# Kernel tuning notes

Hardware: AMD Instinct MI355X
Metric: run time of the kernel (lower is better)

The kernel has to match this reference:

```python
import jax, jax.numpy as jnp
import numpy as np

B, T, N, E = 4, 8, 512, 8192
CIN, H, HEADS = 64, 128, 4


def setup_inputs() -> dict:
    key = jax.random.key(0)
    ks = jax.random.split(key, 8)
    G = B * T
    s = 0.05
    return {
        "x": jax.random.normal(ks[0], (G, N, CIN), jnp.float32),
        "edge_index": jax.random.randint(ks[1], (G, 2, E), 0, N, dtype=jnp.int64),
        "W1": jax.random.normal(ks[2], (CIN, H), jnp.float32) * s,
        "b1": jnp.zeros((H,), jnp.float32),
        "W2": jax.random.normal(ks[3], (H, H), jnp.float32) * s,
        "b2": jnp.zeros((H,), jnp.float32),
        "in_proj_w": jax.random.normal(ks[4], (3 * H, H), jnp.float32) * s,
        "in_proj_b": jnp.zeros((3 * H,), jnp.float32),
        "out_proj_w": jax.random.normal(ks[5], (H, H), jnp.float32) * s,
        "out_proj_b": jnp.zeros((H,), jnp.float32),
    }


def gcn_layer(x, src, dst, W, b, num_nodes):
    # PyG GCNConv: add self-loops, sym-normalize deg^-1/2[src]*deg^-1/2[dst]
    xl = x @ W                                            # [GN, H]
    deg = jax.ops.segment_sum(jnp.ones_like(dst, dtype=xl.dtype), dst,
                              num_segments=num_nodes) + 1.0  # +1 self-loop
    dinv = jax.lax.rsqrt(deg)
    norm = dinv[src] * dinv[dst]                          # [Etot]
    agg = jax.ops.segment_sum(xl[src] * norm[:, None], dst, num_segments=num_nodes)
    agg = agg + xl * (dinv * dinv)[:, None]               # self-loop term
    return agg + b


def reference(x, edge_index, W1, b1, W2, b2, in_proj_w, in_proj_b, out_proj_w, out_proj_b):
    G, n, cin = x.shape
    GN = G * n
    offs = (jnp.arange(G, dtype=edge_index.dtype) * n)[:, None]  # disjoint union
    src = (edge_index[:, 0, :] + offs).reshape(-1)
    dst = (edge_index[:, 1, :] + offs).reshape(-1)
    xf = x.reshape(GN, cin)
    h = gcn_layer(xf, src, dst, W1, b1, GN)
    h = gcn_layer(h, src, dst, W2, b2, GN)
    hc = h.shape[-1]
    h = h.reshape(B, T * n, hc)                           # [B, S, H]
    # torch.nn.MultiheadAttention with packed qkv in_proj
    qkv = h @ in_proj_w.T + in_proj_b
    q, k, v = jnp.split(qkv, 3, axis=-1)
    hd = hc // HEADS
    def sh(t):
        return t.reshape(B, -1, HEADS, hd).transpose(0, 2, 1, 3)  # [B,h,S,d]
    q, k, v = sh(q), sh(k), sh(v)
    att = jax.nn.softmax(jnp.einsum('bhqd,bhkd->bhqk', q, k) / jnp.sqrt(jnp.float32(hd)), axis=-1)
    o = jnp.einsum('bhqk,bhkd->bhqd', att, v).transpose(0, 2, 1, 3).reshape(B, -1, hc)
    return o @ out_proj_w.T + out_proj_b
```

## Files before the change

### kernel.cpp

```cpp
#include <hip/hip_runtime.h>
#include <hip/hip_bf16.h>

#define G     32
#define NPG   512
#define EPG   8192
#define GN    16384
#define ETOT  (G*EPG)
#define CIN   64
#define H     128
#define NB    4
#define S     4096
#define HEADS 4
#define HD    32
#define QKV   384

typedef __attribute__((ext_vector_type(8))) short short8;
typedef __attribute__((ext_vector_type(4))) float floatx4;

__device__ __forceinline__ float bf16_to_f32(unsigned short u) {
    unsigned int x = ((unsigned int)u) << 16;
    return __uint_as_float(x);
}
__device__ __forceinline__ unsigned short f32_to_bf16(float f) {
    __hip_bfloat16 h = (__hip_bfloat16)f;
    return *(unsigned short*)&h;
}
__device__ __forceinline__ float ldf(const void* p, long i, int f32) {
    return f32 ? ((const float*)p)[i] : bf16_to_f32(((const unsigned short*)p)[i]);
}

__global__ void detect_kernel(const unsigned short* __restrict__ xraw,
                              const int* __restrict__ eiraw, int* __restrict__ flags) {
    __shared__ float smax[256];
    __shared__ int   sor[256];
    int t = threadIdx.x;
    float m = 0.f;
    for (int i = t; i < 4096; i += 256)
        m = fmaxf(m, fabsf(bf16_to_f32(xraw[i])));
    int orv = 0;
    for (int i = t; i < 2048; i += 256)
        orv |= eiraw[2 * i + 1];
    smax[t] = m; sor[t] = orv;
    __syncthreads();
    for (int off = 128; off > 0; off >>= 1) {
        if (t < off) {
            smax[t] = fmaxf(smax[t], smax[t + off]);
            sor[t] |= sor[t + off];
        }
        __syncthreads();
    }
    if (t == 0) {
        flags[0] = (smax[0] > 1000.f) ? 1 : 0;
        flags[1] = (sor[0] == 0) ? 1 : 0;
    }
}

#define XN   (GN*CIN)
#define E1   (XN + H*CIN)
#define E2   (E1 + H*H)
#define E3   (E2 + QKV*H)
#define E4   (E3 + H*H)
#define E5   (E4 + H)
#define E6   (E5 + H)
#define E7   (E6 + QKV)
#define CTOT (E7 + H)
__global__ void conv_all_kernel(const void* x_raw, const void* W1_raw, const void* b1_raw,
                                const void* W2_raw, const void* b2_raw, const void* Wq_raw,
                                const void* bq_raw, const void* Wo_raw, const void* bo_raw,
                                unsigned short* __restrict__ xb,
                                unsigned short* __restrict__ W1T,
                                unsigned short* __restrict__ W2T,
                                unsigned short* __restrict__ Wqb,
                                unsigned short* __restrict__ Wob,
                                float* __restrict__ b1f, float* __restrict__ b2f,
                                float* __restrict__ bqf, float* __restrict__ bof,
                                const int* __restrict__ flags) {
    int i = blockIdx.x * blockDim.x + threadIdx.x;
    if (i >= CTOT) return;
    int f32 = flags[0];
    if (i < XN) {
        xb[i] = f32_to_bf16(ldf(x_raw, i, f32));
    } else if (i < E1) {
        int j = i - XN, c = j / CIN, r = j - c * CIN;
        W1T[j] = f32_to_bf16(ldf(W1_raw, (long)r * H + c, f32));
    } else if (i < E2) {
        int j = i - E1, c = j >> 7, r = j & 127;
        W2T[j] = f32_to_bf16(ldf(W2_raw, (long)r * H + c, f32));
    } else if (i < E3) {
        int j = i - E2;
        Wqb[j] = f32_to_bf16(ldf(Wq_raw, j, f32));
    } else if (i < E4) {
        int j = i - E3;
        Wob[j] = f32_to_bf16(ldf(Wo_raw, j, f32));
    } else if (i < E5) { b1f[i - E4] = ldf(b1_raw, i - E4, f32); }
    else if (i < E6) { b2f[i - E5] = ldf(b2_raw, i - E5, f32); }
    else if (i < E7) { bqf[i - E6] = ldf(bq_raw, i - E6, f32); }
    else             { bof[i - E7] = ldf(bo_raw, i - E7, f32); }
}

__global__ void edges_kernel(const int* __restrict__ ei, int* __restrict__ srcA,
                             int* __restrict__ dstA, const int* __restrict__ flags) {
    int t = blockIdx.x * blockDim.x + threadIdx.x;
    if (t >= ETOT) return;
    int g = t >> 13, e = t & (EPG - 1);
    int sh = flags[1];
    long long si = ((long long)(g * 2 + 0) * EPG + e) << sh;
    long long di = ((long long)(g * 2 + 1) * EPG + e) << sh;
    srcA[t] = g * NPG + ei[si];
    dstA[t] = g * NPG + ei[di];
}

__global__ void count_kernel(const int* __restrict__ dstA, int* __restrict__ cnt) {
    int t = blockIdx.x * blockDim.x + threadIdx.x;
    if (t >= ETOT) return;
    atomicAdd(&cnt[dstA[t]], 1);
}

__global__ void scan_kernel(const int* __restrict__ cnt, int* __restrict__ row_start,
                            int* __restrict__ fill_pos, float* __restrict__ dinv) {
    __shared__ int tmp[NPG];
    int g = blockIdx.x, t = threadIdx.x;
    int c = cnt[g * NPG + t];
    tmp[t] = c;
    __syncthreads();
    for (int off = 1; off < NPG; off <<= 1) {
        int v = (t >= off) ? tmp[t - off] : 0;
        __syncthreads();
        tmp[t] += v;
        __syncthreads();
    }
    int excl = tmp[t] - c;
    int rs = g * EPG + excl;
    row_start[g * NPG + t] = rs;
    fill_pos[g * NPG + t]  = rs;
    dinv[g * NPG + t] = 1.0f / sqrtf((float)c + 1.0f);
}

__global__ void fill_kernel(const int* __restrict__ srcA, const int* __restrict__ dstA,
                            int* __restrict__ fill_pos, int* __restrict__ csr_src) {
    int t = blockIdx.x * blockDim.x + threadIdx.x;
    if (t >= ETOT) return;
    int pos = atomicAdd(&fill_pos[dstA[t]], 1);
    csr_src[pos] = srcA[t];
}

template<int KD>
__global__ __launch_bounds__(256) void mm_gcn_kernel(const unsigned short* __restrict__ A,
        const unsigned short* __restrict__ B, const float* __restrict__ dinv,
        unsigned short* __restrict__ Y) {
    int tid = threadIdx.x, wave = tid >> 6, lane = tid & 63, m = lane & 15, quad = lane >> 4;
    int row0 = blockIdx.x * 64 + wave * 16;
    floatx4 acc[8] = {};
    for (int kc = 0; kc < KD; kc += 32) {
        short8 af = *(const short8*)&A[(size_t)(row0 + m) * KD + kc + quad * 8];
#pragma unroll
        for (int t = 0; t < 8; t++) {
            short8 bf = *(const short8*)&B[(size_t)(t * 16 + m) * KD + kc + quad * 8];
            acc[t] = __builtin_amdgcn_mfma_f32_16x16x32_bf16(af, bf, acc[t], 0, 0, 0);
        }
    }
    int rbase = row0 + quad * 4;
    float4 dv4 = *(const float4*)&dinv[rbase];
    float dv[4] = {dv4.x, dv4.y, dv4.z, dv4.w};
#pragma unroll
    for (int t = 0; t < 8; t++) {
        int col = t * 16 + m;
#pragma unroll
        for (int r = 0; r < 4; r++)
            Y[(size_t)(rbase + r) * H + col] = f32_to_bf16(acc[t][r] * dv[r]);
    }
}

__global__ void agg_kernel(const unsigned short* __restrict__ y,
                           const int* __restrict__ row_start, const int* __restrict__ cnt,
                           const int* __restrict__ csr_src, const float* __restrict__ dinv,
                           const float* __restrict__ bias, unsigned short* __restrict__ hout) {
    int i = blockIdx.x;
    int c = threadIdx.x;
    float acc = bf16_to_f32(y[(size_t)i * H + c]);
    int rs = row_start[i], n = cnt[i];
    int p = 0;
    for (; p + 4 <= n; p += 4) {
        int s0 = csr_src[rs + p + 0];
        int s1 = csr_src[rs + p + 1];
        int s2 = csr_src[rs + p + 2];
        int s3 = csr_src[rs + p + 3];
        float a0 = bf16_to_f32(y[(size_t)s0 * H + c]);
        float a1 = bf16_to_f32(y[(size_t)s1 * H + c]);
        float a2 = bf16_to_f32(y[(size_t)s2 * H + c]);
        float a3 = bf16_to_f32(y[(size_t)s3 * H + c]);
        acc += (a0 + a1) + (a2 + a3);
    }
    for (; p < n; p++)
        acc += bf16_to_f32(y[(size_t)csr_src[rs + p] * H + c]);
    hout[(size_t)i * H + c] = f32_to_bf16(acc * dinv[i] + bias[c]);
}

__global__ __launch_bounds__(256) void mmqkv_kernel(const unsigned short* __restrict__ A,
        const unsigned short* __restrict__ B, const float* __restrict__ bias,
        unsigned short* __restrict__ Qx, unsigned short* __restrict__ Kx,
        unsigned short* __restrict__ Vtx) {
    int tid = threadIdx.x, wave = tid >> 6, lane = tid & 63, m = lane & 15, quad = lane >> 4;
    int row0 = blockIdx.x * 64 + wave * 16;
    floatx4 acc[24] = {};
    for (int kc = 0; kc < H; kc += 32) {
        short8 af = *(const short8*)&A[(size_t)(row0 + m) * H + kc + quad * 8];
#pragma unroll
        for (int t = 0; t < 24; t++) {
            short8 bf = *(const short8*)&B[(size_t)(t * 16 + m) * H + kc + quad * 8];
            acc[t] = __builtin_amdgcn_mfma_f32_16x16x32_bf16(af, bf, acc[t], 0, 0, 0);
        }
    }
    int rbase = row0 + quad * 4;
    int b = rbase >> 12, s0 = rbase & (S - 1);
#pragma unroll
    for (int t = 0; t < 24; t++) {
        int j = t * 16 + m;
        float bj = bias[j];
        int jj = j & 127, head = jj >> 5, hd = jj & 31;
        int bh = b * HEADS + head;
        if (t < 8) {
#pragma unroll
            for (int r = 0; r < 4; r++)
                Qx[((size_t)bh * S + s0 + r) * HD + hd] =
                    f32_to_bf16((acc[t][r] + bj) *
                                (0.17677669529663687f * 1.4426950408889634f));
        } else if (t < 16) {
#pragma unroll
            for (int r = 0; r < 4; r++)
                Kx[((size_t)bh * S + s0 + r) * HD + hd] = f32_to_bf16(acc[t][r] + bj);
        } else {
#pragma unroll
            for (int r = 0; r < 4; r++)
                Vtx[((size_t)bh * HD + hd) * S + s0 + r] = f32_to_bf16(acc[t][r] + bj);
        }
    }
}

__global__ __launch_bounds__(256) void attn7_kernel(
        const unsigned short* __restrict__ Qx, const unsigned short* __restrict__ Kx,
        const unsigned short* __restrict__ Vtx, unsigned short* __restrict__ Ob) {
    int tid = threadIdx.x, wave = tid >> 6, lane = tid & 63;
    int m = lane & 15, quad = lane >> 4;

    int n = blockIdx.x;
    int id = (n & 7) * 32 + (n >> 3);
    int tile = id & 15, bh = id >> 4;

    const unsigned short* Qb  = Qx  + (size_t)bh * S * HD;
    const unsigned short* Kb  = Kx  + (size_t)bh * S * HD;
    const unsigned short* Vtb = Vtx + (size_t)bh * HD * S;

    int q0 = tile * 256 + wave * 64;
    short8 q[4];
#pragma unroll
    for (int t = 0; t < 4; t++)
        q[t] = *(const short8*)&Qb[(size_t)(q0 + t * 16 + m) * HD + quad * 8];

    floatx4 o0[4] = {}, o1[4] = {}, l[4] = {};

    short8 ones = {16256, 16256, 16256, 16256, 16256, 16256, 16256, 16256};
    union PW { unsigned int u[4]; short8 s8; };

    short8 kf0 = *(const short8*)&Kb[(size_t)m * HD + quad * 8];
    short8 kf1 = *(const short8*)&Kb[(size_t)(m + 16) * HD + quad * 8];
    short8 vc0 = *(const short8*)&Vtb[(size_t)m * S + quad * 8];
    short8 vc1 = *(const short8*)&Vtb[(size_t)(m + 16) * S + quad * 8];

    for (int i = 0; i < S / 32; i++) {
        floatx4 z = {};
        floatx4 t0[4], t1[4];
#pragma unroll
        for (int t = 0; t < 4; t++) {
            t0[t] = __builtin_amdgcn_mfma_f32_16x16x32_bf16(kf0, q[t], z, 0, 0, 0);
            t1[t] = __builtin_amdgcn_mfma_f32_16x16x32_bf16(kf1, q[t], z, 0, 0, 0);
        }
        int ktn = ((i + 1) * 32) & (S - 1);
        kf0 = *(const short8*)&Kb[(size_t)(ktn + m) * HD + quad * 8];
        kf1 = *(const short8*)&Kb[(size_t)(ktn + m + 16) * HD + quad * 8];

        PW pw[4];
#pragma unroll
        for (int t = 0; t < 4; t++) {
            float e0 = __builtin_amdgcn_exp2f(t0[t][0]);
            float e1 = __builtin_amdgcn_exp2f(t0[t][1]);
            float e2 = __builtin_amdgcn_exp2f(t0[t][2]);
            float e3 = __builtin_amdgcn_exp2f(t0[t][3]);
            float e4 = __builtin_amdgcn_exp2f(t1[t][0]);
            float e5 = __builtin_amdgcn_exp2f(t1[t][1]);
            float e6 = __builtin_amdgcn_exp2f(t1[t][2]);
            float e7 = __builtin_amdgcn_exp2f(t1[t][3]);
            unsigned int w0, w1, w2, w3;
            asm("v_cvt_pk_bf16_f32 %0, %1, %2" : "=v"(w0) : "v"(e0), "v"(e1));
            asm("v_cvt_pk_bf16_f32 %0, %1, %2" : "=v"(w1) : "v"(e2), "v"(e3));
            asm("v_cvt_pk_bf16_f32 %0, %1, %2" : "=v"(w2) : "v"(e4), "v"(e5));
            asm("v_cvt_pk_bf16_f32 %0, %1, %2" : "=v"(w3) : "v"(e6), "v"(e7));
            asm("v_permlane32_swap_b32 %0, %1" : "+v"(w0), "+v"(w2));
            asm("v_permlane32_swap_b32 %0, %1" : "+v"(w1), "+v"(w3));
            asm("v_permlane16_swap_b32 %0, %1" : "+v"(w0), "+v"(w2));
            asm("v_permlane16_swap_b32 %0, %1" : "+v"(w1), "+v"(w3));
            pw[t].u[0] = w0; pw[t].u[1] = w1; pw[t].u[2] = w2; pw[t].u[3] = w3;
        }

#pragma unroll
        for (int t = 0; t < 4; t++) {
            o0[t] = __builtin_amdgcn_mfma_f32_16x16x32_bf16(pw[t].s8, vc0, o0[t], 0, 0, 0);
            o1[t] = __builtin_amdgcn_mfma_f32_16x16x32_bf16(pw[t].s8, vc1, o1[t], 0, 0, 0);
            l[t]  = __builtin_amdgcn_mfma_f32_16x16x32_bf16(pw[t].s8, ones, l[t], 0, 0, 0);
        }
        vc0 = *(const short8*)&Vtb[(size_t)m * S + ktn + quad * 8];
        vc1 = *(const short8*)&Vtb[(size_t)(m + 16) * S + ktn + quad * 8];
    }

    int batch = bh >> 2, head = bh & 3;
    int col = head * HD + m;
#pragma unroll
    for (int t = 0; t < 4; t++) {
        int grow = batch * S + q0 + t * 16 + quad * 4;
#pragma unroll
        for (int r = 0; r < 4; r++) {
            float inv = 1.f / l[t][r];
            Ob[(size_t)(grow + r) * H + col]      = f32_to_bf16(o0[t][r] * inv);
            Ob[(size_t)(grow + r) * H + col + 16] = f32_to_bf16(o1[t][r] * inv);
        }
    }
}

__global__ __launch_bounds__(256) void mmout_kernel(const unsigned short* __restrict__ A,
        const unsigned short* __restrict__ B, const float* __restrict__ bias,
        void* __restrict__ out, const int* __restrict__ flags) {
    int tid = threadIdx.x, wave = tid >> 6, lane = tid & 63, m = lane & 15, quad = lane >> 4;
    int row0 = blockIdx.x * 64 + wave * 16;
    floatx4 acc[8] = {};
    for (int kc = 0; kc < H; kc += 32) {
        short8 af = *(const short8*)&A[(size_t)(row0 + m) * H + kc + quad * 8];
#pragma unroll
        for (int t = 0; t < 8; t++) {
            short8 bf = *(const short8*)&B[(size_t)(t * 16 + m) * H + kc + quad * 8];
            acc[t] = __builtin_amdgcn_mfma_f32_16x16x32_bf16(af, bf, acc[t], 0, 0, 0);
        }
    }
    int rbase = row0 + quad * 4;
    int f32o = flags[0];
#pragma unroll
    for (int t = 0; t < 8; t++) {
        int col = t * 16 + m;
        float bj = bias[col];
#pragma unroll
        for (int r = 0; r < 4; r++) {
            float v = acc[t][r] + bj;
            if (f32o) ((float*)out)[(size_t)(rbase + r) * H + col] = v;
            else ((unsigned short*)out)[(size_t)(rbase + r) * H + col] = f32_to_bf16(v);
        }
    }
}

extern "C" void kernel_launch(void* const* d_in, const int* in_sizes, int n_in,
                              void* d_out, int out_size, void* d_ws, size_t ws_size,
                              hipStream_t stream) {
    const void* x_raw    = d_in[0];
    const int*  ei_raw   = (const int*)d_in[1];
    const void* W1_raw   = d_in[2];
    const void* b1_raw   = d_in[3];
    const void* W2_raw   = d_in[4];
    const void* b2_raw   = d_in[5];
    const void* Wq_raw   = d_in[6];
    const void* bq_raw   = d_in[7];
    const void* Wo_raw   = d_in[8];
    const void* bo_raw   = d_in[9];

    char* ws = (char*)d_ws;
    size_t o = 0;
    auto alloc = [&](size_t bytes) { void* p = ws + o; o += (bytes + 1023) & ~1023ull; return p; };

    int*   flags     = (int*)  alloc(1024);
    int*   cnt       = (int*)  alloc((size_t)GN * 4);
    int*   row_start = (int*)  alloc((size_t)GN * 4);
    int*   fill_pos  = (int*)  alloc((size_t)GN * 4);
    float* dinv      = (float*)alloc((size_t)GN * 4);
    int*   srcA      = (int*)  alloc((size_t)ETOT * 4);
    int*   dstA      = (int*)  alloc((size_t)ETOT * 4);
    int*   csr_src   = (int*)  alloc((size_t)ETOT * 4);
    unsigned short* xb   = (unsigned short*)alloc((size_t)GN * CIN * 2);
    unsigned short* W1T  = (unsigned short*)alloc((size_t)H * CIN * 2);
    unsigned short* W2T  = (unsigned short*)alloc((size_t)H * H * 2);
    unsigned short* Wqb  = (unsigned short*)alloc((size_t)QKV * H * 2);
    unsigned short* Wob  = (unsigned short*)alloc((size_t)H * H * 2);
    float* b1f = (float*)alloc(H * 4);
    float* b2f = (float*)alloc(H * 4);
    float* bqf = (float*)alloc(QKV * 4);
    float* bof = (float*)alloc(H * 4);
    unsigned short* y_bf = (unsigned short*)alloc((size_t)GN * H * 2);
    unsigned short* h_bf = (unsigned short*)alloc((size_t)GN * H * 2);
    unsigned short* Qx   = (unsigned short*)alloc((size_t)16 * S * HD * 2);
    unsigned short* Kx   = (unsigned short*)alloc((size_t)16 * S * HD * 2);
    unsigned short* Vtx  = (unsigned short*)alloc((size_t)16 * S * HD * 2);
    unsigned short* Obf  = y_bf;

    detect_kernel<<<1, 256, 0, stream>>>((const unsigned short*)x_raw, ei_raw, flags);

    conv_all_kernel<<<(CTOT + 255) / 256, 256, 0, stream>>>(
        x_raw, W1_raw, b1_raw, W2_raw, b2_raw, Wq_raw, bq_raw, Wo_raw, bo_raw,
        xb, W1T, W2T, Wqb, Wob, b1f, b2f, bqf, bof, flags);

    edges_kernel<<<ETOT / 256, 256, 0, stream>>>(ei_raw, srcA, dstA, flags);
    hipMemsetAsync(cnt, 0, (size_t)GN * 4, stream);
    count_kernel<<<ETOT / 256, 256, 0, stream>>>(dstA, cnt);
    scan_kernel<<<G, NPG, 0, stream>>>(cnt, row_start, fill_pos, dinv);
    fill_kernel<<<ETOT / 256, 256, 0, stream>>>(srcA, dstA, fill_pos, csr_src);

    mm_gcn_kernel<CIN><<<GN / 64, 256, 0, stream>>>(xb, W1T, dinv, y_bf);
    agg_kernel<<<GN, H, 0, stream>>>(y_bf, row_start, cnt, csr_src, dinv, b1f, h_bf);
    mm_gcn_kernel<H><<<GN / 64, 256, 0, stream>>>(h_bf, W2T, dinv, y_bf);
    agg_kernel<<<GN, H, 0, stream>>>(y_bf, row_start, cnt, csr_src, dinv, b2f, h_bf);

    mmqkv_kernel<<<GN / 64, 256, 0, stream>>>(h_bf, Wqb, bqf, Qx, Kx, Vtx);
    attn7_kernel<<<dim3(256), 256, 0, stream>>>(Qx, Kx, Vtx, Obf);
    mmout_kernel<<<GN / 64, 256, 0, stream>>>(Obf, Wob, bof, d_out, flags);
}
```

Baseline: 270.0 us.

## Aggregate layer-1 in 64-wide input space before matmul; fuse edge count

Uses linearity of GCN to aggregate the pre-scaled 64-channel input features before multiplying by W1, halving the gathered width for the first layer's sparse aggregation. The dinv source scaling is folded into the input conversion, and a new bias-only matmul applies W1 after aggregation. Edge extraction and degree counting are merged into one kernel, removing a launch and a reread of dstA. This reorders launches so the CSR scan runs before conversion, and it changes bf16 rounding points.

Result: faster. 258.3 us (-4.3%).

```diff
diff --git a/kernel.cpp b/kernel.cpp
--- a/kernel.cpp
+++ b/kernel.cpp
@@ -74,12 +74,13 @@
                                 unsigned short* __restrict__ Wob,
                                 float* __restrict__ b1f, float* __restrict__ b2f,
                                 float* __restrict__ bqf, float* __restrict__ bof,
+                                const float* __restrict__ dinv,
                                 const int* __restrict__ flags) {
     int i = blockIdx.x * blockDim.x + threadIdx.x;
     if (i >= CTOT) return;
     int f32 = flags[0];
     if (i < XN) {
-        xb[i] = f32_to_bf16(ldf(x_raw, i, f32));
+        xb[i] = f32_to_bf16(ldf(x_raw, i, f32) * dinv[i >> 6]);
     } else if (i < E1) {
         int j = i - XN, c = j / CIN, r = j - c * CIN;
         W1T[j] = f32_to_bf16(ldf(W1_raw, (long)r * H + c, f32));
@@ -98,22 +99,20 @@
     else             { bof[i - E7] = ldf(bo_raw, i - E7, f32); }
 }
 
-__global__ void edges_kernel(const int* __restrict__ ei, int* __restrict__ srcA,
-                             int* __restrict__ dstA, const int* __restrict__ flags) {
+__global__ void edges_count_kernel(const int* __restrict__ ei, int* __restrict__ srcA,
+                                   int* __restrict__ dstA, int* __restrict__ cnt,
+                                   const int* __restrict__ flags) {
     int t = blockIdx.x * blockDim.x + threadIdx.x;
     if (t >= ETOT) return;
     int g = t >> 13, e = t & (EPG - 1);
     int sh = flags[1];
     long long si = ((long long)(g * 2 + 0) * EPG + e) << sh;
     long long di = ((long long)(g * 2 + 1) * EPG + e) << sh;
-    srcA[t] = g * NPG + ei[si];
-    dstA[t] = g * NPG + ei[di];
-}
-
-__global__ void count_kernel(const int* __restrict__ dstA, int* __restrict__ cnt) {
-    int t = blockIdx.x * blockDim.x + threadIdx.x;
-    if (t >= ETOT) return;
-    atomicAdd(&cnt[dstA[t]], 1);
+    int s = g * NPG + ei[si];
+    int d = g * NPG + ei[di];
+    srcA[t] = s;
+    dstA[t] = d;
+    atomicAdd(&cnt[d], 1);
 }
 
 __global__ void scan_kernel(const int* __restrict__ cnt, int* __restrict__ row_start,
@@ -142,6 +141,57 @@
     if (t >= ETOT) return;
     int pos = atomicAdd(&fill_pos[dstA[t]], 1);
     csr_src[pos] = srcA[t];
+}
+
+__global__ void agg64_kernel(const unsigned short* __restrict__ xb,
+                             const int* __restrict__ row_start, const int* __restrict__ cnt,
+                             const int* __restrict__ csr_src, const float* __restrict__ dinv,
+                             unsigned short* __restrict__ z) {
+    int i = blockIdx.x;
+    int c = threadIdx.x;
+    float acc = bf16_to_f32(xb[(size_t)i * CIN + c]);
+    int rs = row_start[i], n = cnt[i];
+    int p = 0;
+    for (; p + 4 <= n; p += 4) {
+        int s0 = csr_src[rs + p + 0];
+        int s1 = csr_src[rs + p + 1];
+        int s2 = csr_src[rs + p + 2];
+        int s3 = csr_src[rs + p + 3];
+        float a0 = bf16_to_f32(xb[(size_t)s0 * CIN + c]);
+        float a1 = bf16_to_f32(xb[(size_t)s1 * CIN + c]);
+        float a2 = bf16_to_f32(xb[(size_t)s2 * CIN + c]);
+        float a3 = bf16_to_f32(xb[(size_t)s3 * CIN + c]);
+        acc += (a0 + a1) + (a2 + a3);
+    }
+    for (; p < n; p++)
+        acc += bf16_to_f32(xb[(size_t)csr_src[rs + p] * CIN + c]);
+    z[(size_t)i * CIN + c] = f32_to_bf16(acc * dinv[i]);
+}
+
+template<int KD>
+__global__ __launch_bounds__(256) void mm_bias_kernel(const unsigned short* __restrict__ A,
+        const unsigned short* __restrict__ B, const float* __restrict__ bias,
+        unsigned short* __restrict__ Y) {
+    int tid = threadIdx.x, wave = tid >> 6, lane = tid & 63, m = lane & 15, quad = lane >> 4;
+    int row0 = blockIdx.x * 64 + wave * 16;
+    floatx4 acc[8] = {};
+    for (int kc = 0; kc < KD; kc += 32) {
+        short8 af = *(const short8*)&A[(size_t)(row0 + m) * KD + kc + quad * 8];
+#pragma unroll
+        for (int t = 0; t < 8; t++) {
+            short8 bf = *(const short8*)&B[(size_t)(t * 16 + m) * KD + kc + quad * 8];
+            acc[t] = __builtin_amdgcn_mfma_f32_16x16x32_bf16(af, bf, acc[t], 0, 0, 0);
+        }
+    }
+    int rbase = row0 + quad * 4;
+#pragma unroll
+    for (int t = 0; t < 8; t++) {
+        int col = t * 16 + m;
+        float bj = bias[col];
+#pragma unroll
+        for (int r = 0; r < 4; r++)
+            Y[(size_t)(rbase + r) * H + col] = f32_to_bf16(acc[t][r] + bj);
+    }
 }
 
 template<int KD>
@@ -382,6 +432,7 @@
     int*   dstA      = (int*)  alloc((size_t)ETOT * 4);
     int*   csr_src   = (int*)  alloc((size_t)ETOT * 4);
     unsigned short* xb   = (unsigned short*)alloc((size_t)GN * CIN * 2);
+    unsigned short* zb   = (unsigned short*)alloc((size_t)GN * CIN * 2);
     unsigned short* W1T  = (unsigned short*)alloc((size_t)H * CIN * 2);
     unsigned short* W2T  = (unsigned short*)alloc((size_t)H * H * 2);
     unsigned short* Wqb  = (unsigned short*)alloc((size_t)QKV * H * 2);
@@ -399,18 +450,18 @@
 
     detect_kernel<<<1, 256, 0, stream>>>((const unsigned short*)x_raw, ei_raw, flags);
 
+    hipMemsetAsync(cnt, 0, (size_t)GN * 4, stream);
+    edges_count_kernel<<<ETOT / 256, 256, 0, stream>>>(ei_raw, srcA, dstA, cnt, flags);
+    scan_kernel<<<G, NPG, 0, stream>>>(cnt, row_start, fill_pos, dinv);
+
     conv_all_kernel<<<(CTOT + 255) / 256, 256, 0, stream>>>(
         x_raw, W1_raw, b1_raw, W2_raw, b2_raw, Wq_raw, bq_raw, Wo_raw, bo_raw,
-        xb, W1T, W2T, Wqb, Wob, b1f, b2f, bqf, bof, flags);
-
-    edges_kernel<<<ETOT / 256, 256, 0, stream>>>(ei_raw, srcA, dstA, flags);
-    hipMemsetAsync(cnt, 0, (size_t)GN * 4, stream);
-    count_kernel<<<ETOT / 256, 256, 0, stream>>>(dstA, cnt);
-    scan_kernel<<<G, NPG, 0, stream>>>(cnt, row_start, fill_pos, dinv);
+        xb, W1T, W2T, Wqb, Wob, b1f, b2f, bqf, bof, dinv, flags);
+
     fill_kernel<<<ETOT / 256, 256, 0, stream>>>(srcA, dstA, fill_pos, csr_src);
 
-    mm_gcn_kernel<CIN><<<GN / 64, 256, 0, stream>>>(xb, W1T, dinv, y_bf);
-    agg_kernel<<<GN, H, 0, stream>>>(y_bf, row_start, cnt, csr_src, dinv, b1f, h_bf);
+    agg64_kernel<<<GN, CIN, 0, stream>>>(xb, row_start, cnt, csr_src, dinv, zb);
+    mm_bias_kernel<CIN><<<GN / 64, 256, 0, stream>>>(zb, W1T, b1f, h_bf);
     mm_gcn_kernel<H><<<GN / 64, 256, 0, stream>>>(h_bf, W2T, dinv, y_bf);
     agg_kernel<<<GN, H, 0, stream>>>(y_bf, row_start, cnt, csr_src, dinv, b2f, h_bf);
 
```
